# Optimization experiments

Hardware: AMD Instinct MI355X
Metric: run time of the kernel (lower is better)

## Reference

```python
import jax, jax.numpy as jnp
import numpy as np

B = 1024
N_SPEC = 2048
R1 = 20000
R2 = 40000


def setup_inputs() -> dict:
    key = jax.random.key(0)
    k1, k2, k3, k4, k5, k6, k7 = jax.random.split(key, 7)
    return {
        "y_in": jax.random.uniform(k1, (B, N_SPEC), dtype=jnp.float32),
        "rates_1st": jax.random.uniform(k2, (B, R1), dtype=jnp.float32),
        "rates_2nd": jax.random.uniform(k3, (B, R2), dtype=jnp.float32),
        "inds_1r": jax.random.randint(k4, (R1,), 0, N_SPEC, dtype=jnp.int32),
        "inds_1p": jax.random.randint(k5, (R1,), 0, N_SPEC, dtype=jnp.int32),
        "inds_2r": jax.random.randint(k6, (R2, 2), 0, N_SPEC, dtype=jnp.int32),
        "inds_2p": jax.random.randint(k7, (R2,), 0, N_SPEC, dtype=jnp.int32),
    }


def reference(y_in, rates_1st, rates_2nd, inds_1r, inds_1p, inds_2r, inds_2p):
    # First-order reactions: gather reactant abundance, scale by rate,
    # scatter-add into product species.  y_in: [B, S]
    term_1 = y_in[:, inds_1r] * rates_1st                      # [B, R1]
    # Second-order reactions: product of the two reactant abundances.
    term_2 = y_in[:, inds_2r[:, 0]] * y_in[:, inds_2r[:, 1]] * rates_2nd  # [B, R2]
    y_out = jnp.zeros_like(y_in)
    y_out = y_out.at[:, inds_1p].add(term_1)
    y_out = y_out.at[:, inds_2p].add(term_2)
    return y_out
```

## Files before the change

kernel.cpp:

```cpp
#include <hip/hip_runtime.h>


#define NSPEC 2048
#define BDIM  1024
#define R1    20000
#define R2    40000
#define CH    4000
#define NCH1  (R1 / CH)
#define NCH2  (R2 / CH)
#define NCH   (NCH1 + NCH2)

#define WS_PTRR 0
#define WS_PERM (NCH * NSPEC * 4)
#define WS_E    (WS_PERM + NCH * NSPEC * 2)

__global__ __launch_bounds__(1024) void k_build(
    const int* __restrict__ inds_1p, const int* __restrict__ inds_2p,
    uint* __restrict__ ptrr, ushort* __restrict__ perm, ushort* __restrict__ e)
{
    __shared__ uint cnt[NSPEC];
    __shared__ uint part[1024];
    __shared__ uint h2[64];
    __shared__ uint off[64];

    const int c   = blockIdx.x;
    const int tid = threadIdx.x;

    cnt[tid] = 0u; cnt[tid + 1024] = 0u;
    __syncthreads();

    const bool first = (c < NCH1);
    const int* __restrict__ prod = first ? (inds_1p + c * CH)
                                         : (inds_2p + (c - NCH1) * CH);

    for (int i = tid; i < CH; i += 1024)
        atomicAdd(&cnt[prod[i]], 1u);
    __syncthreads();

    uint v0 = cnt[2 * tid], v1 = cnt[2 * tid + 1];
    uint tsum = v0 + v1;
    part[tid] = tsum;
    __syncthreads();
    for (int o = 1; o < 1024; o <<= 1) {
        uint x = (tid >= o) ? part[tid - o] : 0u;
        __syncthreads();
        part[tid] += x;
        __syncthreads();
    }
    const uint run  = part[tid] - tsum;
    const uint beg0 = run, beg1 = run + v0;
    cnt[2 * tid]     = beg0;
    cnt[2 * tid + 1] = beg1;
    if (tid < 64) h2[tid] = 0u;
    __syncthreads();

    ushort* ec = e + c * CH;
    for (int i = tid; i < CH; i += 1024) {
        const int s = prod[i];
        const uint pos = atomicAdd(&cnt[s], 1u);
        ec[pos] = (ushort)i;
    }
    const uint b0 = min(v0, 63u), b1 = min(v1, 63u);
    atomicAdd(&h2[b0], 1u);
    atomicAdd(&h2[b1], 1u);
    __syncthreads();

    if (tid == 0) {
        uint a = 0;
        for (int v = 63; v >= 0; --v) { off[v] = a; a += h2[v]; }
    }
    __syncthreads();

    const uint r0 = atomicAdd(&off[b0], 1u);
    const uint r1 = atomicAdd(&off[b1], 1u);
    perm[c * NSPEC + r0] = (ushort)(2 * tid);
    perm[c * NSPEC + r1] = (ushort)(2 * tid + 1);
    ptrr[c * NSPEC + r0] = beg0 | (v0 << 16);
    ptrr[c * NSPEC + r1] = beg1 | (v1 << 16);
}

#define MBLOCK 512

__global__ __launch_bounds__(MBLOCK, 8) void k_main(
    const float* __restrict__ y_in,
    const float* __restrict__ rates_1st,
    const float* __restrict__ rates_2nd,
    const int*   __restrict__ inds_1r,
    const int*   __restrict__ inds_2r,
    const uint*  __restrict__ ptrr,
    const ushort* __restrict__ perm,
    const ushort* __restrict__ e,
    float*       __restrict__ y_out)
{
    __shared__ float  ys[NSPEC];
    __shared__ float  accl[NSPEC];
    __shared__ float  tl[CH];
    __shared__ ushort el[CH];

    const int b   = blockIdx.x;
    const int tid = threadIdx.x;

    ((float4*)ys)[tid] = ((const float4*)(y_in + (size_t)b * NSPEC))[tid];
    accl[tid]        = 0.f;
    accl[tid + 512]  = 0.f;
    accl[tid + 1024] = 0.f;
    accl[tid + 1536] = 0.f;
    __syncthreads();

    for (int c = 0; c < NCH; ++c) {
        if (c < NCH1) {
            const int base = c * CH;
            const int4*   iv = (const int4*)  (inds_1r + base);
            const float4* rv = (const float4*)(rates_1st + (size_t)b * R1 + base);
            for (int i = tid; i < CH / 4; i += MBLOCK) {
                const int4   r = iv[i];
                const float4 q = rv[i];
                float4 t;
                t.x = ys[r.x] * q.x;
                t.y = ys[r.y] * q.y;
                t.z = ys[r.z] * q.z;
                t.w = ys[r.w] * q.w;
                ((float4*)tl)[i] = t;
            }
        } else {
            const int base = (c - NCH1) * CH;
            const uint4*  iv = (const uint4*) (inds_2r + 2 * base);
            const float2* rv = (const float2*)(rates_2nd + (size_t)b * R2 + base);
            for (int i = tid; i < CH / 2; i += MBLOCK) {
                const uint4  r = iv[i];
                const float2 q = rv[i];
                float2 t;
                t.x = ys[r.x] * ys[r.y] * q.x;
                t.y = ys[r.z] * ys[r.w] * q.y;
                ((float2*)tl)[i] = t;
            }
        }
        {
            const uint4* sv = (const uint4*)(e + c * CH);
            for (int i = tid; i < (CH * 2) / 16; i += MBLOCK)
                ((uint4*)el)[i] = sv[i];
        }
        __syncthreads();

        const uint*   pr = ptrr + c * NSPEC;
        const ushort* pm = perm + c * NSPEC;
        #pragma unroll
        for (int k = 0; k < 4; ++k) {
            const int  rank = k * MBLOCK + tid;
            const uint bc   = pr[rank];
            const int  s    = pm[rank];
            uint j = bc & 0xFFFFu;
            uint n = bc >> 16;
            float a = 0.f;
            for (; n > 0; --n, ++j) a += tl[el[j]];
            accl[s] += a;
        }
        __syncthreads();
    }

    ((float4*)(y_out + (size_t)b * NSPEC))[tid] = ((const float4*)accl)[tid];
}

extern "C" void kernel_launch(void* const* d_in, const int* in_sizes, int n_in,
                              void* d_out, int out_size, void* d_ws, size_t ws_size,
                              hipStream_t stream) {
    const float* y_in      = (const float*)d_in[0];
    const float* rates_1st = (const float*)d_in[1];
    const float* rates_2nd = (const float*)d_in[2];
    const int*   inds_1r   = (const int*)d_in[3];
    const int*   inds_1p   = (const int*)d_in[4];
    const int*   inds_2r   = (const int*)d_in[5];
    const int*   inds_2p   = (const int*)d_in[6];
    float*       y_out     = (float*)d_out;

    char* ws = (char*)d_ws;
    uint*   ptrr = (uint*)  (ws + WS_PTRR);
    ushort* perm = (ushort*)(ws + WS_PERM);
    ushort* e    = (ushort*)(ws + WS_E);

    k_build<<<NCH, 1024, 0, stream>>>(inds_1p, inds_2p, ptrr, perm, e);
    k_main<<<BDIM, MBLOCK, 0, stream>>>(y_in, rates_1st, rates_2nd,
                                        inds_1r, inds_2r, ptrr, perm, e, y_out);
}
```

Before: 341.8 us.

## Scatter reaction terms directly into sorted order, dropping the indirect edge list

The per-chunk term buffer is now written in product-sorted order during the gather phase, with the destination slot precomputed in the build kernel and packed with the reactant index for first-order chunks. The reduction phase then sums contiguous runs instead of reading an indirection array. Run start, count and species are packed into a single word, which removes the separate perm load, and the chunk size grows to 5000 so there are fewer chunk iterations and barriers. In exchange the LDS writes become scattered, which can cause bank conflicts. Packing the count into 8 bits clamps any run longer than 255, which would silently drop terms.

Result: faster. 331.8 us (-2.9%).

```diff
diff --git a/kernel.cpp b/kernel.cpp
--- a/kernel.cpp
+++ b/kernel.cpp
@@ -5,18 +5,19 @@
 #define BDIM  1024
 #define R1    20000
 #define R2    40000
-#define CH    4000
+#define CH    5000
 #define NCH1  (R1 / CH)
 #define NCH2  (R2 / CH)
 #define NCH   (NCH1 + NCH2)
 
 #define WS_PTRR 0
-#define WS_PERM (NCH * NSPEC * 4)
-#define WS_E    (WS_PERM + NCH * NSPEC * 2)
+#define WS_E1P  (NCH * NSPEC * 4)
+#define WS_CSR2 (WS_E1P + R1 * 4)
 
 __global__ __launch_bounds__(1024) void k_build(
+    const int* __restrict__ inds_1r,
     const int* __restrict__ inds_1p, const int* __restrict__ inds_2p,
-    uint* __restrict__ ptrr, ushort* __restrict__ perm, ushort* __restrict__ e)
+    uint* __restrict__ ptrr, uint* __restrict__ e1p, ushort* __restrict__ csr2)
 {
     __shared__ uint cnt[NSPEC];
     __shared__ uint part[1024];
@@ -30,8 +31,8 @@
     __syncthreads();
 
     const bool first = (c < NCH1);
-    const int* __restrict__ prod = first ? (inds_1p + c * CH)
-                                         : (inds_2p + (c - NCH1) * CH);
+    const int  base  = first ? c * CH : (c - NCH1) * CH;
+    const int* __restrict__ prod = first ? (inds_1p + base) : (inds_2p + base);
 
     for (int i = tid; i < CH; i += 1024)
         atomicAdd(&cnt[prod[i]], 1u);
@@ -54,11 +55,18 @@
     if (tid < 64) h2[tid] = 0u;
     __syncthreads();
 
-    ushort* ec = e + c * CH;
-    for (int i = tid; i < CH; i += 1024) {
-        const int s = prod[i];
-        const uint pos = atomicAdd(&cnt[s], 1u);
-        ec[pos] = (ushort)i;
+    if (first) {
+        for (int i = tid; i < CH; i += 1024) {
+            const int s = prod[i];
+            const uint pos = atomicAdd(&cnt[s], 1u);
+            e1p[c * CH + i] = (uint)inds_1r[base + i] | (pos << 11);
+        }
+    } else {
+        for (int i = tid; i < CH; i += 1024) {
+            const int s = prod[i];
+            const uint pos = atomicAdd(&cnt[s], 1u);
+            csr2[base + i] = (ushort)pos;
+        }
     }
     const uint b0 = min(v0, 63u), b1 = min(v1, 63u);
     atomicAdd(&h2[b0], 1u);
@@ -73,10 +81,8 @@
 
     const uint r0 = atomicAdd(&off[b0], 1u);
     const uint r1 = atomicAdd(&off[b1], 1u);
-    perm[c * NSPEC + r0] = (ushort)(2 * tid);
-    perm[c * NSPEC + r1] = (ushort)(2 * tid + 1);
-    ptrr[c * NSPEC + r0] = beg0 | (v0 << 16);
-    ptrr[c * NSPEC + r1] = beg1 | (v1 << 16);
+    ptrr[c * NSPEC + r0] = beg0 | (min(v0, 255u) << 13) | ((uint)(2 * tid) << 21);
+    ptrr[c * NSPEC + r1] = beg1 | (min(v1, 255u) << 13) | ((uint)(2 * tid + 1) << 21);
 }
 
 #define MBLOCK 512
@@ -85,74 +91,62 @@
     const float* __restrict__ y_in,
     const float* __restrict__ rates_1st,
     const float* __restrict__ rates_2nd,
-    const int*   __restrict__ inds_1r,
     const int*   __restrict__ inds_2r,
     const uint*  __restrict__ ptrr,
-    const ushort* __restrict__ perm,
-    const ushort* __restrict__ e,
+    const uint*  __restrict__ e1p,
+    const ushort* __restrict__ csr2,
     float*       __restrict__ y_out)
 {
-    __shared__ float  ys[NSPEC];
-    __shared__ float  accl[NSPEC];
-    __shared__ float  tl[CH];
-    __shared__ ushort el[CH];
+    __shared__ float ys[NSPEC];
+    __shared__ float accl[NSPEC];
+    __shared__ float tl[CH];
 
     const int b   = blockIdx.x;
     const int tid = threadIdx.x;
 
     ((float4*)ys)[tid] = ((const float4*)(y_in + (size_t)b * NSPEC))[tid];
-    accl[tid]        = 0.f;
-    accl[tid + 512]  = 0.f;
-    accl[tid + 1024] = 0.f;
-    accl[tid + 1536] = 0.f;
+    ((float4*)accl)[tid] = make_float4(0.f, 0.f, 0.f, 0.f);
     __syncthreads();
 
     for (int c = 0; c < NCH; ++c) {
         if (c < NCH1) {
-            const int base = c * CH;
-            const int4*   iv = (const int4*)  (inds_1r + base);
-            const float4* rv = (const float4*)(rates_1st + (size_t)b * R1 + base);
+            const uint4*  ev = (const uint4*) (e1p + c * CH);
+            const float4* rv = (const float4*)(rates_1st + (size_t)b * R1 + c * CH);
             for (int i = tid; i < CH / 4; i += MBLOCK) {
-                const int4   r = iv[i];
+                const uint4  e = ev[i];
                 const float4 q = rv[i];
-                float4 t;
-                t.x = ys[r.x] * q.x;
-                t.y = ys[r.y] * q.y;
-                t.z = ys[r.z] * q.z;
-                t.w = ys[r.w] * q.w;
-                ((float4*)tl)[i] = t;
+                tl[e.x >> 11] = ys[e.x & 2047u] * q.x;
+                tl[e.y >> 11] = ys[e.y & 2047u] * q.y;
+                tl[e.z >> 11] = ys[e.z & 2047u] * q.z;
+                tl[e.w >> 11] = ys[e.w & 2047u] * q.w;
             }
         } else {
-            const int base = (c - NCH1) * CH;
-            const uint4*  iv = (const uint4*) (inds_2r + 2 * base);
-            const float2* rv = (const float2*)(rates_2nd + (size_t)b * R2 + base);
-            for (int i = tid; i < CH / 2; i += MBLOCK) {
-                const uint4  r = iv[i];
-                const float2 q = rv[i];
-                float2 t;
-                t.x = ys[r.x] * ys[r.y] * q.x;
-                t.y = ys[r.z] * ys[r.w] * q.y;
-                ((float2*)tl)[i] = t;
+            const int c2 = c - NCH1;
+            const uint4*   iv = (const uint4*)  (inds_2r + 2 * (c2 * CH));
+            const float4*  rv = (const float4*) (rates_2nd + (size_t)b * R2 + c2 * CH);
+            const ushort4* pv = (const ushort4*)(csr2 + c2 * CH);
+            for (int i = tid; i < CH / 4; i += MBLOCK) {
+                const uint4   ia = iv[2 * i];
+                const uint4   ib = iv[2 * i + 1];
+                const float4  q  = rv[i];
+                const ushort4 p  = pv[i];
+                tl[p.x] = ys[ia.x] * ys[ia.y] * q.x;
+                tl[p.y] = ys[ia.z] * ys[ia.w] * q.y;
+                tl[p.z] = ys[ib.x] * ys[ib.y] * q.z;
+                tl[p.w] = ys[ib.z] * ys[ib.w] * q.w;
             }
-        }
-        {
-            const uint4* sv = (const uint4*)(e + c * CH);
-            for (int i = tid; i < (CH * 2) / 16; i += MBLOCK)
-                ((uint4*)el)[i] = sv[i];
         }
         __syncthreads();
 
-        const uint*   pr = ptrr + c * NSPEC;
-        const ushort* pm = perm + c * NSPEC;
+        const uint* pr = ptrr + c * NSPEC;
         #pragma unroll
         for (int k = 0; k < 4; ++k) {
-            const int  rank = k * MBLOCK + tid;
-            const uint bc   = pr[rank];
-            const int  s    = pm[rank];
-            uint j = bc & 0xFFFFu;
-            uint n = bc >> 16;
+            const uint v   = pr[k * MBLOCK + tid];
+            uint       j   = v & 0x1FFFu;
+            uint       n   = (v >> 13) & 0xFFu;
+            const uint s   = v >> 21;
             float a = 0.f;
-            for (; n > 0; --n, ++j) a += tl[el[j]];
+            for (; n > 0; --n, ++j) a += tl[j];
             accl[s] += a;
         }
         __syncthreads();
@@ -175,10 +169,10 @@
 
     char* ws = (char*)d_ws;
     uint*   ptrr = (uint*)  (ws + WS_PTRR);
-    ushort* perm = (ushort*)(ws + WS_PERM);
-    ushort* e    = (ushort*)(ws + WS_E);
+    uint*   e1p  = (uint*)  (ws + WS_E1P);
+    ushort* csr2 = (ushort*)(ws + WS_CSR2);
 
-    k_build<<<NCH, 1024, 0, stream>>>(inds_1p, inds_2p, ptrr, perm, e);
-    k_main<<<BDIM, MBLOCK, 0, stream>>>(y_in, rates_1st, rates_2nd,
-                                        inds_1r, inds_2r, ptrr, perm, e, y_out);
+    k_build<<<NCH, 1024, 0, stream>>>(inds_1r, inds_1p, inds_2p, ptrr, e1p, csr2);
+    k_main<<<BDIM, MBLOCK, 0, stream>>>(y_in, rates_1st, rates_2nd, inds_2r,
+                                        ptrr, e1p, csr2, y_out);
 }
```
